# Kernel tuning notes

Measured on AMD Instinct MI355X. Metric: run time of the kernel, lower is better.

Reference implementation:

```python
import jax, jax.numpy as jnp
import numpy as np

NH, NL, NPNT = 8, 4, 4          # heads, levels, points
NQ, BS, NK, D, DFFN = 100, 8, 18, 256, 1024
SPATIAL = np.array([[92, 92], [46, 46], [23, 23], [12, 12]], np.int32)
LEN_MEM = int((SPATIAL[:, 0] * SPATIAL[:, 1]).sum())  # 11253


def _layernorm(x, g, b):
    m = x.mean(-1, keepdims=True)
    v = ((x - m) ** 2).mean(-1, keepdims=True)
    return (x - m) / jnp.sqrt(v + 1e-5) * g + b


def _mha(xq, xk, xv, in_w, in_b, out_w, out_b):
    # torch nn.MultiheadAttention semantics, inputs (S, B, D)
    S, B, d = xq.shape
    dh = d // NH
    wq, wk, wv = jnp.split(in_w, 3, axis=0)
    bq, bk, bv = jnp.split(in_b, 3, axis=0)
    def proj(x, w, b):
        return (x @ w.T + b).reshape(x.shape[0], B, NH, dh).transpose(1, 2, 0, 3)
    q = proj(xq, wq, bq) * (1.0 / np.sqrt(dh))
    k = proj(xk, wk, bk)
    v = proj(xv, wv, bv)
    att = jax.nn.softmax(jnp.einsum('bhqd,bhkd->bhqk', q, k), axis=-1)
    o = jnp.einsum('bhqk,bhkd->bhqd', att, v).transpose(2, 0, 1, 3).reshape(S, B, d)
    return o @ out_w.T + out_b


def _bilinear(v_l, loc):
    # v_l: (bs,H,W,NH,dh); loc: (bs,Lq,NH,P,2) normalized [0,1]
    # matches F.grid_sample(align_corners=False, padding_mode='zeros')
    bs, H, W, nh, dh = v_l.shape
    x = loc[..., 0] * W - 0.5
    y = loc[..., 1] * H - 0.5
    x0 = jnp.floor(x); y0 = jnp.floor(y)
    lx = x - x0; ly = y - y0
    b_idx = jnp.arange(bs)[:, None, None, None]
    h_idx = jnp.arange(nh)[None, None, :, None]
    def corner(xa, ya, w):
        valid = (xa >= 0) & (xa < W) & (ya >= 0) & (ya < H)
        xi = jnp.clip(xa, 0, W - 1).astype(jnp.int32)
        yi = jnp.clip(ya, 0, H - 1).astype(jnp.int32)
        return v_l[b_idx, yi, xi, h_idx] * (w * valid)[..., None]
    return (corner(x0, y0, (1 - lx) * (1 - ly)) + corner(x0 + 1, y0, lx * (1 - ly))
            + corner(x0, y0 + 1, (1 - lx) * ly) + corner(x0 + 1, y0 + 1, lx * ly))


def _msda(q, rp, mem, pad_mask, ss, off_w, off_b, aw_w, aw_b, val_w, val_b, outp_w, outp_b):
    bs, Lq, d = q.shape
    dh = d // NH
    value = mem @ val_w.T + val_b
    value = jnp.where(pad_mask[..., None], 0.0, value).reshape(bs, -1, NH, dh)
    off = (q @ off_w.T + off_b).reshape(bs, Lq, NH, NL, NPNT, 2)
    aw = jax.nn.softmax((q @ aw_w.T + aw_b).reshape(bs, Lq, NH, NL * NPNT), -1)
    aw = aw.reshape(bs, Lq, NH, NL, NPNT)
    wh = jnp.asarray(ss[:, ::-1].copy(), jnp.float32)  # offset normalizer (W, H)
    loc = rp[:, :, None, :, None, :] + off / wh[None, None, None, :, None, :]
    out = jnp.zeros((bs, Lq, NH, dh), q.dtype)
    start = 0
    for l in range(NL):
        H, W = int(ss[l, 0]), int(ss[l, 1])
        v_l = value[:, start:start + H * W].reshape(bs, H, W, NH, dh)
        start += H * W
        samp = _bilinear(v_l, loc[:, :, :, l])          # (bs,Lq,NH,P,dh)
        out = out + (samp * aw[:, :, :, l, :, None]).sum(3)
    return out.reshape(bs, Lq, d) @ outp_w.T + outp_b


def _forward(tgt_pose, pos, ref_points, memory, w_in_w, w_in_b, w_out_w, w_out_b,
             a_in_w, a_in_b, a_out_w, a_out_b, off_w, off_b, aw_w, aw_b,
             val_w, val_b, outp_w, outp_b, wn_g, wn_b, an_g, an_b,
             n1_g, n1_b, n2_g, n2_b, l1_w, l1_b, l2_w, l2_b,
             spatial_shapes, level_start_index, padding_mask):
    ss = np.asarray(jax.device_get(spatial_shapes))
    nq, bs, nk, d = tgt_pose.shape
    # within-group self-attn over the nk keypoint tokens.
    # NOTE: with_pos_embed mutates tgt_pose in place in the torch code, so
    # q = k = v = tgt + pos and the residual also uses tgt + pos (faithful).
    t = tgt_pose + pos
    x = t.reshape(nq * bs, nk, d).transpose(1, 0, 2)   # (nk, nq*bs, d)
    a1 = _mha(x, x, x, w_in_w, w_in_b, w_out_w, w_out_b)
    t = _layernorm(t + a1.transpose(1, 0, 2).reshape(nq, bs, nk, d), wn_g, wn_b)
    # across-group self-attn over the nq groups
    x2 = t.reshape(nq, bs * nk, d)
    a2 = _mha(x2, x2, x2, a_in_w, a_in_b, a_out_w, a_out_b)
    t = _layernorm(t + a2.reshape(nq, bs, nk, d), an_g, an_b)
    # MSDeformAttn cross-attention (in-place pos add again, faithful)
    t = t + pos
    q = t.transpose(1, 0, 2, 3).reshape(bs, nq * nk, d)
    rp = jnp.swapaxes(ref_points, 0, 1)                # (bs, nq*nk, NL, 2)
    mem = jnp.swapaxes(memory, 0, 1)                   # (bs, LEN_MEM, d)
    c = _msda(q, rp, mem, padding_mask, ss, off_w, off_b, aw_w, aw_b,
              val_w, val_b, outp_w, outp_b)
    c = c.reshape(bs, nq, nk, d).transpose(1, 0, 2, 3)
    t = _layernorm(t + c, n1_g, n1_b)
    # FFN (dropout is identity in eval)
    h = jax.nn.relu(t @ l1_w.T + l1_b)
    return _layernorm(t + (h @ l2_w.T + l2_b), n2_g, n2_b)


def setup_inputs() -> dict:
    key = jax.random.key(0)
    ks = jax.random.split(key, 16)
    p = lambda k, shape: jax.random.normal(k, shape, jnp.float32) * 0.02
    lsi = np.concatenate([[0], np.cumsum(SPATIAL[:, 0] * SPATIAL[:, 1])[:-1]]).astype(np.int32)
    return {
        'tgt_pose': jax.random.normal(ks[0], (NQ, BS, NK, D), jnp.float32),
        'pos': jax.random.normal(ks[1], (NQ, BS, NK, D), jnp.float32),
        'ref_points': jax.random.uniform(ks[2], (NQ * NK, BS, NL, 2), jnp.float32),
        'memory': jax.random.normal(ks[3], (LEN_MEM, BS, D), jnp.float32),
        'w_in_w': p(ks[4], (3 * D, D)), 'w_in_b': jnp.zeros((3 * D,)),
        'w_out_w': p(ks[5], (D, D)), 'w_out_b': jnp.zeros((D,)),
        'a_in_w': p(ks[6], (3 * D, D)), 'a_in_b': jnp.zeros((3 * D,)),
        'a_out_w': p(ks[7], (D, D)), 'a_out_b': jnp.zeros((D,)),
        'off_w': p(ks[8], (NH * NL * NPNT * 2, D)),
        'off_b': jax.random.uniform(ks[9], (NH * NL * NPNT * 2,), jnp.float32, -2.0, 2.0),
        'aw_w': p(ks[10], (NH * NL * NPNT, D)), 'aw_b': jnp.zeros((NH * NL * NPNT,)),
        'val_w': p(ks[11], (D, D)), 'val_b': jnp.zeros((D,)),
        'outp_w': p(ks[12], (D, D)), 'outp_b': jnp.zeros((D,)),
        'wn_g': jnp.ones((D,)), 'wn_b': jnp.zeros((D,)),
        'an_g': jnp.ones((D,)), 'an_b': jnp.zeros((D,)),
        'n1_g': jnp.ones((D,)), 'n1_b': jnp.zeros((D,)),
        'n2_g': jnp.ones((D,)), 'n2_b': jnp.zeros((D,)),
        'l1_w': p(ks[13], (DFFN, D)), 'l1_b': jnp.zeros((DFFN,)),
        'l2_w': p(ks[14], (D, DFFN)), 'l2_b': jnp.zeros((D,)),
        'spatial_shapes': jnp.asarray(SPATIAL),
        'level_start_index': jnp.asarray(lsi),
        'padding_mask': jnp.zeros((BS, LEN_MEM), bool),
    }


def reference(tgt_pose, pos, ref_points, memory, w_in_w, w_in_b, w_out_w, w_out_b,
              a_in_w, a_in_b, a_out_w, a_out_b, off_w, off_b, aw_w, aw_b,
              val_w, val_b, outp_w, outp_b, wn_g, wn_b, an_g, an_b,
              n1_g, n1_b, n2_g, n2_b, l1_w, l1_b, l2_w, l2_b,
              spatial_shapes, level_start_index, padding_mask):
    return _forward(tgt_pose, pos, ref_points, memory, w_in_w, w_in_b, w_out_w, w_out_b,
                    a_in_w, a_in_b, a_out_w, a_out_b, off_w, off_b, aw_w, aw_b,
                    val_w, val_b, outp_w, outp_b, wn_g, wn_b, an_g, an_b,
                    n1_g, n1_b, n2_g, n2_b, l1_w, l1_b, l2_w, l2_b,
                    spatial_shapes, level_start_index, padding_mask)
```

## Files before the change

### kernel.cpp

```cpp
#include <hip/hip_runtime.h>
#include <math.h>

#define NH_ 8
#define D_ 256
#define NK_ 18
#define NQ_ 100
#define BS_ 8
#define LQ_ 1800
#define LEN_MEM_ 11253
#define NTOK_ 14400

typedef short bf16x8 __attribute__((ext_vector_type(8)));
typedef float f32x4 __attribute__((ext_vector_type(4)));
typedef unsigned short ushort;

__device__ inline ushort f2bf(float f) {
    unsigned int u = __builtin_bit_cast(unsigned int, f);
    unsigned int r = (u + 0x7fffu + ((u >> 16) & 1u)) >> 16;
    return (ushort)r;
}
__device__ inline float bf2f(unsigned int u16) {
    unsigned int i = u16 << 16;
    return __builtin_bit_cast(float, i);
}
__device__ inline int packbf2(float a, float b) {
    return (int)f2bf(a) | ((int)f2bf(b) << 16);
}

__global__ __launch_bounds__(256)
void wcvt_kernel(const float* s0, const float* s1, const float* s2, const float* s3,
                 const float* s4, const float* s5, const float* s6, const float* s7,
                 const float* s8, const float* s9, ushort* dst) {
    const int sizes[10] = {196608,65536,196608,65536,65536,32768,65536,65536,262144,262144};
    const int offs[10]  = {0,196608,262144,458752,524288,589824,622592,688128,753664,1015808};
    int ti = blockIdx.y;
    const float* s;
    switch (ti) {
        case 0: s = s0; break; case 1: s = s1; break; case 2: s = s2; break;
        case 3: s = s3; break; case 4: s = s4; break; case 5: s = s5; break;
        case 6: s = s6; break; case 7: s = s7; break; case 8: s = s8; break;
        default: s = s9; break;
    }
    int n = sizes[ti];
    int i = (blockIdx.x * 256 + threadIdx.x) * 8;
    if (i >= n) return;
    ushort* d = dst + offs[ti] + i;
    float4 f0 = *(const float4*)(s + i);
    float4 f1 = *(const float4*)(s + i + 4);
    int4 val;
    val.x = packbf2(f0.x, f0.y);
    val.y = packbf2(f0.z, f0.w);
    val.z = packbf2(f1.x, f1.y);
    val.w = packbf2(f1.z, f1.w);
    *(int4*)d = val;
}

__global__ __launch_bounds__(256)
void addcvt_kernel(const float* __restrict__ a, const float* __restrict__ b,
                   float* __restrict__ c, ushort* __restrict__ cbf, int n4) {
    int i = blockIdx.x * blockDim.x + threadIdx.x;
    if (i >= n4) return;
    float4 av = ((const float4*)a)[i];
    float4 bv = ((const float4*)b)[i];
    float4 cv;
    cv.x = av.x + bv.x; cv.y = av.y + bv.y; cv.z = av.z + bv.z; cv.w = av.w + bv.w;
    ((float4*)c)[i] = cv;
    uint2 p;
    p.x = (unsigned int)packbf2(cv.x, cv.y);
    p.y = (unsigned int)packbf2(cv.z, cv.w);
    *(uint2*)(cbf + (size_t)i * 4) = p;
}

template<int MODE, bool RELU, bool A_F32, bool OUT_BF16>
__global__ __launch_bounds__(256)
void gemm_kernel(const void* __restrict__ Av, const ushort* __restrict__ W,
                 const float* __restrict__ bias, void* __restrict__ Cv,
                 int M, int N, int K, const unsigned char* __restrict__ mask) {
    constexpr int AST = 72;
    __shared__ ushort As[128 * AST];
    __shared__ ushort Bs[128 * AST];
    const int m0 = blockIdx.x * 128, n0 = blockIdx.y * 128;
    const int tid = threadIdx.x;
    const int w = tid >> 6, lane = tid & 63;
    const int wr = w >> 1, wc = w & 1;
    const int fr = lane & 15, hi = lane >> 4;
    f32x4 acc[4][4];
#pragma unroll
    for (int i = 0; i < 4; ++i)
#pragma unroll
        for (int j = 0; j < 4; ++j) acc[i][j] = f32x4{0.f, 0.f, 0.f, 0.f};

    const int srow = tid >> 1, shalf = tid & 1;
    long arow = 0;
    const bool avalid = (m0 + srow) < M;
    {
        int gr = m0 + srow;
        if (gr >= M) gr = M - 1;
        if (MODE == 2) {
            int b = gr / LQ_; int lq = gr - b * LQ_;
            int q = lq / NK_; int kk = lq - q * NK_;
            arow = (long)q * (BS_ * NK_) + b * NK_ + kk;
        } else {
            arow = gr;
        }
    }

    for (int k0 = 0; k0 < K; k0 += 64) {
        ushort* ad = As + srow * AST + shalf * 32;
        if (avalid) {
            if (A_F32) {
                const float* ap = (const float*)Av + arow * (long)K + k0 + shalf * 32;
#pragma unroll
                for (int i = 0; i < 4; ++i) {
                    float4 f0 = *(const float4*)(ap + i * 8);
                    float4 f1 = *(const float4*)(ap + i * 8 + 4);
                    int4 v;
                    v.x = packbf2(f0.x, f0.y); v.y = packbf2(f0.z, f0.w);
                    v.z = packbf2(f1.x, f1.y); v.w = packbf2(f1.z, f1.w);
                    *(int4*)(ad + i * 8) = v;
                }
            } else {
                const ushort* ap = (const ushort*)Av + arow * (long)K + k0 + shalf * 32;
#pragma unroll
                for (int i = 0; i < 4; ++i) *(int4*)(ad + i * 8) = *(const int4*)(ap + i * 8);
            }
        } else {
            int4 z = make_int4(0, 0, 0, 0);
#pragma unroll
            for (int i = 0; i < 4; ++i) *(int4*)(ad + i * 8) = z;
        }
        {
            const ushort* wp = W + (long)(n0 + srow) * K + k0 + shalf * 32;
            ushort* bd = Bs + srow * AST + shalf * 32;
#pragma unroll
            for (int i = 0; i < 4; ++i) *(int4*)(bd + i * 8) = *(const int4*)(wp + i * 8);
        }
        __syncthreads();
#pragma unroll
        for (int kb = 0; kb < 2; ++kb) {
            bf16x8 af[4], bfr[4];
#pragma unroll
            for (int i = 0; i < 4; ++i)
                af[i] = *(const bf16x8*)(As + (wr * 64 + i * 16 + fr) * AST + kb * 32 + hi * 8);
#pragma unroll
            for (int j = 0; j < 4; ++j)
                bfr[j] = *(const bf16x8*)(Bs + (wc * 64 + j * 16 + fr) * AST + kb * 32 + hi * 8);
#pragma unroll
            for (int i = 0; i < 4; ++i)
#pragma unroll
                for (int j = 0; j < 4; ++j)
                    acc[i][j] = __builtin_amdgcn_mfma_f32_16x16x32_bf16(af[i], bfr[j], acc[i][j], 0, 0, 0);
        }
        __syncthreads();
    }

#pragma unroll
    for (int i = 0; i < 4; ++i) {
#pragma unroll
        for (int r = 0; r < 4; ++r) {
            int gm = m0 + wr * 64 + i * 16 + hi * 4 + r;
            if (gm >= M) continue;
            long orow = gm;
            bool zero = false;
            if (MODE == 1) {
                if (mask && mask[(size_t)(gm & 7) * LEN_MEM_ + (gm >> 3)]) zero = true;
            } else if (MODE == 3) {
                int b = gm / LQ_; int lq = gm - b * LQ_;
                int q = lq / NK_; int kk = lq - q * NK_;
                orow = (long)q * (BS_ * NK_) + b * NK_ + kk;
            }
#pragma unroll
            for (int j = 0; j < 4; ++j) {
                int gn = n0 + wc * 64 + j * 16 + fr;
                float v = acc[i][j][r] + bias[gn];
                if (RELU) v = fmaxf(v, 0.f);
                if (zero) v = 0.f;
                if (OUT_BF16) ((ushort*)Cv)[orow * (long)N + gn] = f2bf(v);
                else ((float*)Cv)[orow * (long)N + gn] = v;
            }
        }
    }
}

template<int S, int SP, int HPB>
__global__ __launch_bounds__(256)
void mattn_kernel(const ushort* __restrict__ qkv, ushort* __restrict__ outb,
                  int rsG, int rsS) {
    constexpr int SPk = ((SP + 31) / 32) * 32;
    constexpr int KST = 40;
    constexpr int PST = SPk + 8;
    constexpr int NT = SP / 16;
    constexpr int NB = HPB * NT;
    constexpr int HB = 8 / HPB;
    __shared__ ushort KsA[HPB * SP * KST];
    __shared__ ushort VtA[HPB * 32 * PST];
    __shared__ ushort PA [HPB * SP * PST];

    const int tid = threadIdx.x;
    const int g = blockIdx.x / HB;
    const int hbase = (blockIdx.x % HB) * HPB;

    for (int idx = tid; idx < HPB * S * 4; idx += 256) {
        int hh = idx / (S * 4); int rem = idx - hh * (S * 4);
        int j = rem >> 2, q = rem & 3;
        const ushort* base = qkv + ((size_t)g * rsG + (size_t)j * rsS) * 768 + (hbase + hh) * 32 + q * 8;
        uint4 kv = *(const uint4*)(base + 256);
        ushort* kd = KsA + hh * (SP * KST) + j * KST + q * 8;
        *(uint2*)kd = make_uint2(kv.x, kv.y);
        *(uint2*)(kd + 4) = make_uint2(kv.z, kv.w);
        uint4 vv = *(const uint4*)(base + 512);
        ushort* vt = VtA + hh * (32 * PST) + j;
        unsigned int uu[4] = {vv.x, vv.y, vv.z, vv.w};
#pragma unroll
        for (int e = 0; e < 4; ++e) {
            vt[(q * 8 + e * 2    ) * PST] = (ushort)(uu[e] & 0xffff);
            vt[(q * 8 + e * 2 + 1) * PST] = (ushort)(uu[e] >> 16);
        }
    }
    for (int idx = tid; idx < HPB * 32 * (SPk - S); idx += 256) {
        int hh = idx / (32 * (SPk - S)); int rem = idx - hh * (32 * (SPk - S));
        int d = rem / (SPk - S); int c = S + rem - d * (SPk - S);
        VtA[hh * 32 * PST + d * PST + c] = 0;
    }
    if constexpr (SPk > SP) {
        constexpr int PW = SPk - SP;
        for (int idx = tid; idx < HPB * SP * PW; idx += 256) {
            int hh = idx / (SP * PW); int rem = idx - hh * (SP * PW);
            int rrow = rem / PW; int c = SP + rem - rrow * PW;
            PA[hh * SP * PST + rrow * PST + c] = 0;
        }
    }
    __syncthreads();

    const int wv = tid >> 6, lane = tid & 63, fr = lane & 15, hi = lane >> 4;
    for (int band = wv; band < NB; band += 4) {
        const int hh = band / NT, mb = band - (band / NT) * NT;
        const int h = hbase + hh;
        const ushort* Ks = KsA + hh * (SP * KST);
        const ushort* Vt = VtA + hh * (32 * PST);
        ushort* P = PA + hh * (SP * PST);

        int sq = mb * 16 + fr; if (sq > S - 1) sq = S - 1;
        bf16x8 qf = *(const bf16x8*)(qkv + ((size_t)g * rsG + (size_t)sq * rsS) * 768 + h * 32 + hi * 8);
        f32x4 sc[NT];
#pragma unroll
        for (int t = 0; t < NT; ++t) {
            bf16x8 kf = *(const bf16x8*)(Ks + (t * 16 + fr) * KST + hi * 8);
            sc[t] = __builtin_amdgcn_mfma_f32_16x16x32_bf16(qf, kf, f32x4{0.f, 0.f, 0.f, 0.f}, 0, 0, 0);
        }
#pragma unroll
        for (int t = 0; t < NT; ++t) {
            bool valid = (t * 16 + fr) < S;
#pragma unroll
            for (int r = 0; r < 4; ++r)
                sc[t][r] = valid ? sc[t][r] * 0.17677669529663687f : -1e30f;
        }
#pragma unroll
        for (int r = 0; r < 4; ++r) {
            float m = sc[0][r];
#pragma unroll
            for (int t = 1; t < NT; ++t) m = fmaxf(m, sc[t][r]);
            m = fmaxf(m, __shfl_xor(m, 1)); m = fmaxf(m, __shfl_xor(m, 2));
            m = fmaxf(m, __shfl_xor(m, 4)); m = fmaxf(m, __shfl_xor(m, 8));
            float e[NT]; float sum = 0.f;
#pragma unroll
            for (int t = 0; t < NT; ++t) { e[t] = __expf(sc[t][r] - m); sum += e[t]; }
            sum += __shfl_xor(sum, 1); sum += __shfl_xor(sum, 2);
            sum += __shfl_xor(sum, 4); sum += __shfl_xor(sum, 8);
            float inv = 1.f / sum;
            int row = mb * 16 + hi * 4 + r;
#pragma unroll
            for (int t = 0; t < NT; ++t)
                P[row * PST + t * 16 + fr] = f2bf(e[t] * inv);
        }
        f32x4 o0 = {0.f, 0.f, 0.f, 0.f}, o1 = {0.f, 0.f, 0.f, 0.f};
#pragma unroll
        for (int kb = 0; kb < SPk / 32; ++kb) {
            bf16x8 pf = *(const bf16x8*)(P + (mb * 16 + fr) * PST + kb * 32 + hi * 8);
            bf16x8 v0 = *(const bf16x8*)(Vt + fr * PST + kb * 32 + hi * 8);
            bf16x8 v1 = *(const bf16x8*)(Vt + (16 + fr) * PST + kb * 32 + hi * 8);
            o0 = __builtin_amdgcn_mfma_f32_16x16x32_bf16(pf, v0, o0, 0, 0, 0);
            o1 = __builtin_amdgcn_mfma_f32_16x16x32_bf16(pf, v1, o1, 0, 0, 0);
        }
#pragma unroll
        for (int r = 0; r < 4; ++r) {
            int s = mb * 16 + hi * 4 + r;
            if (s < S) {
                size_t ob = ((size_t)g * rsG + (size_t)s * rsS) * 256 + h * 32;
                outb[ob + fr] = f2bf(o0[r]);
                outb[ob + 16 + fr] = f2bf(o1[r]);
            }
        }
    }
}

__global__ __launch_bounds__(256)
void addln_kernel(const float* __restrict__ base, const float* __restrict__ delta,
                  const float* __restrict__ gamma, const float* __restrict__ beta,
                  const float* __restrict__ pos,
                  float* __restrict__ out, ushort* __restrict__ obf, int M) {
    int row = blockIdx.x * 4 + (threadIdx.x >> 6);
    int lane = threadIdx.x & 63;
    if (row >= M) return;
    const float* pb = base + (size_t)row * 256;
    const float* pd = delta + (size_t)row * 256;
    float v[4]; float s = 0.f;
#pragma unroll
    for (int i = 0; i < 4; ++i) { int c = lane + i * 64; v[i] = pb[c] + pd[c]; s += v[i]; }
#pragma unroll
    for (int off = 32; off; off >>= 1) s += __shfl_xor(s, off);
    float mean = s * (1.f / 256.f);
    float var = 0.f;
#pragma unroll
    for (int i = 0; i < 4; ++i) { float d = v[i] - mean; var += d * d; }
#pragma unroll
    for (int off = 32; off; off >>= 1) var += __shfl_xor(var, off);
    var *= (1.f / 256.f);
    float rstd = rsqrtf(var + 1e-5f);
#pragma unroll
    for (int i = 0; i < 4; ++i) {
        int c = lane + i * 64;
        float o = (v[i] - mean) * rstd * gamma[c] + beta[c];
        if (pos) o += pos[(size_t)row * 256 + c];
        out[(size_t)row * 256 + c] = o;
        if (obf) obf[(size_t)row * 256 + c] = f2bf(o);
    }
}

__global__ __launch_bounds__(256)
void msda_kernel(const float* __restrict__ offb, const float* __restrict__ aw,
                 const ushort* __restrict__ val, const float* __restrict__ refp,
                 const int* __restrict__ spatial, const int* __restrict__ lsi,
                 ushort* __restrict__ samp) {
    int unit = blockIdx.x * 16 + (threadIdx.x >> 4);
    int lane = threadIdx.x & 15;
    int lbase = (threadIdx.x & 63) & 48;
    int h = unit & 7;
    int t = unit >> 3;
    int lq = t % LQ_;
    int b = t / LQ_;

    float logit = aw[((size_t)b * LQ_ + lq) * 128 + h * 16 + lane];
    float m = logit;
    m = fmaxf(m, __shfl_xor(m, 1)); m = fmaxf(m, __shfl_xor(m, 2));
    m = fmaxf(m, __shfl_xor(m, 4)); m = fmaxf(m, __shfl_xor(m, 8));
    float e = __expf(logit - m);
    float sum = e;
    sum += __shfl_xor(sum, 1); sum += __shfl_xor(sum, 2);
    sum += __shfl_xor(sum, 4); sum += __shfl_xor(sum, 8);
    float wnorm = e / sum;

    const float* offp = offb + ((size_t)b * LQ_ + lq) * 256 + h * 32;
    float2 myoff = ((const float2*)offp)[lane];

    float acc0 = 0.f, acc1 = 0.f;
#pragma unroll
    for (int lvl = 0; lvl < 4; ++lvl) {
        int H = spatial[lvl * 2], W = spatial[lvl * 2 + 1];
        int st = lsi[lvl];
        float rpx = refp[(((size_t)lq * BS_ + b) * 4 + lvl) * 2 + 0];
        float rpy = refp[(((size_t)lq * BS_ + b) * 4 + lvl) * 2 + 1];
        const ushort* vb = val + ((size_t)st * 8 + b) * 256 + h * 32 + lane * 2;
        float fW = (float)W, fH = (float)H;
#pragma unroll
        for (int p = 0; p < 4; ++p) {
            int pi = lvl * 4 + p;
            float ox = __shfl(myoff.x, lbase + pi);
            float oy = __shfl(myoff.y, lbase + pi);
            float wpt = __shfl(wnorm, lbase + pi);
            float x = rpx * fW + ox - 0.5f;
            float y = rpy * fH + oy - 0.5f;
            float x0f = floorf(x), y0f = floorf(y);
            float lx = x - x0f, ly = y - y0f;
            int x0 = (int)x0f, y0 = (int)y0f;
            int xc0 = min(max(x0, 0), W - 1), xc1 = min(max(x0 + 1, 0), W - 1);
            int yc0 = min(max(y0, 0), H - 1), yc1 = min(max(y0 + 1, 0), H - 1);
            float vx0 = (x0 >= 0 && x0 < W) ? 1.f : 0.f;
            float vx1 = (x0 >= -1 && x0 + 1 < W) ? 1.f : 0.f;
            float vy0 = (y0 >= 0 && y0 < H) ? 1.f : 0.f;
            float vy1 = (y0 >= -1 && y0 + 1 < H) ? 1.f : 0.f;
            float w00 = wpt * (1.f - lx) * (1.f - ly) * vx0 * vy0;
            float w10 = wpt * lx * (1.f - ly) * vx1 * vy0;
            float w01 = wpt * (1.f - lx) * ly * vx0 * vy1;
            float w11 = wpt * lx * ly * vx1 * vy1;
            unsigned int u00 = *(const unsigned int*)(vb + ((size_t)(yc0 * W + xc0) * 8) * 256);
            unsigned int u10 = *(const unsigned int*)(vb + ((size_t)(yc0 * W + xc1) * 8) * 256);
            unsigned int u01 = *(const unsigned int*)(vb + ((size_t)(yc1 * W + xc0) * 8) * 256);
            unsigned int u11 = *(const unsigned int*)(vb + ((size_t)(yc1 * W + xc1) * 8) * 256);
            acc0 += w00 * bf2f(u00 & 0xffff) + w10 * bf2f(u10 & 0xffff)
                  + w01 * bf2f(u01 & 0xffff) + w11 * bf2f(u11 & 0xffff);
            acc1 += w00 * bf2f(u00 >> 16) + w10 * bf2f(u10 >> 16)
                  + w01 * bf2f(u01 >> 16) + w11 * bf2f(u11 >> 16);
        }
    }
    size_t o = ((size_t)b * LQ_ + lq) * 256 + h * 32 + lane * 2;
    *(unsigned int*)(samp + o) = (unsigned int)packbf2(acc0, acc1);
}

extern "C" void kernel_launch(void* const* d_in, const int* in_sizes, int n_in,
                              void* d_out, int out_size, void* d_ws, size_t ws_size,
                              hipStream_t stream) {
    const float* tgt     = (const float*)d_in[0];
    const float* pos     = (const float*)d_in[1];
    const float* refp    = (const float*)d_in[2];
    const float* memory  = (const float*)d_in[3];
    const float* w_in_w  = (const float*)d_in[4];
    const float* w_in_b  = (const float*)d_in[5];
    const float* w_out_w = (const float*)d_in[6];
    const float* w_out_b = (const float*)d_in[7];
    const float* a_in_w  = (const float*)d_in[8];
    const float* a_in_b  = (const float*)d_in[9];
    const float* a_out_w = (const float*)d_in[10];
    const float* a_out_b = (const float*)d_in[11];
    const float* off_w   = (const float*)d_in[12];
    const float* off_b   = (const float*)d_in[13];
    const float* aw_w    = (const float*)d_in[14];
    const float* aw_b    = (const float*)d_in[15];
    const float* val_w   = (const float*)d_in[16];
    const float* val_b   = (const float*)d_in[17];
    const float* outp_w  = (const float*)d_in[18];
    const float* outp_b  = (const float*)d_in[19];
    const float* wn_g    = (const float*)d_in[20];
    const float* wn_b    = (const float*)d_in[21];
    const float* an_g    = (const float*)d_in[22];
    const float* an_b    = (const float*)d_in[23];
    const float* n1_g    = (const float*)d_in[24];
    const float* n1_b    = (const float*)d_in[25];
    const float* n2_g    = (const float*)d_in[26];
    const float* n2_b    = (const float*)d_in[27];
    const float* l1_w    = (const float*)d_in[28];
    const float* l1_b    = (const float*)d_in[29];
    const float* l2_w    = (const float*)d_in[30];
    const float* l2_b    = (const float*)d_in[31];
    const int*   spatial = (const int*)d_in[32];
    const int*   lsi     = (const int*)d_in[33];
    const unsigned char* pmask = (const unsigned char*)d_in[34];
    float* out = (float*)d_out;

    float*  T      = (float*)d_ws;
    ushort* Tbf    = (ushort*)(T + 3686400);
    ushort* B16    = Tbf + 3686400;
    ushort* CBbf   = B16 + 11059200;
    ushort* VALbf  = CBbf + 3686400;
    ushort* SAMPbf = VALbf + 23046144;
    ushort* Hbf    = SAMPbf + 3686400;
    ushort* WB     = Hbf + 14745600;
    float*  OFF    = (float*)(WB + 1277952);
    float*  AW     = OFF + 3686400;

    ushort* WB_win  = WB + 0;
    ushort* WB_wout = WB + 196608;
    ushort* WB_ain  = WB + 262144;
    ushort* WB_aout = WB + 458752;
    ushort* WB_off  = WB + 524288;
    ushort* WB_aw   = WB + 589824;
    ushort* WB_val  = WB + 622592;
    ushort* WB_outp = WB + 688128;
    ushort* WB_l1   = WB + 753664;
    ushort* WB_l2   = WB + 1015808;

    const int n4 = NTOK_ * 256 / 4;

    wcvt_kernel<<<dim3(128, 10), 256, 0, stream>>>(
        w_in_w, w_out_w, a_in_w, a_out_w, off_w, aw_w, val_w, outp_w, l1_w, l2_w, WB);
    addcvt_kernel<<<n4 / 256, 256, 0, stream>>>(tgt, pos, T, Tbf, n4);
    gemm_kernel<0, false, false, true><<<dim3(113, 6), 256, 0, stream>>>(
        Tbf, WB_win, w_in_b, B16, NTOK_, 768, 256, nullptr);
    mattn_kernel<18, 32, 4><<<800 * 2, 256, 0, stream>>>(B16, CBbf, 18, 1);
    gemm_kernel<0, false, false, false><<<dim3(113, 2), 256, 0, stream>>>(
        CBbf, WB_wout, w_out_b, OFF, NTOK_, 256, 256, nullptr);
    addln_kernel<<<NTOK_ / 4, 256, 0, stream>>>(T, OFF, wn_g, wn_b, nullptr, T, Tbf, NTOK_);
    gemm_kernel<0, false, false, true><<<dim3(113, 6), 256, 0, stream>>>(
        Tbf, WB_ain, a_in_b, B16, NTOK_, 768, 256, nullptr);
    mattn_kernel<100, 112, 1><<<144 * 8, 256, 0, stream>>>(B16, CBbf, 1, 144);
    gemm_kernel<0, false, false, false><<<dim3(113, 2), 256, 0, stream>>>(
        CBbf, WB_aout, a_out_b, OFF, NTOK_, 256, 256, nullptr);
    addln_kernel<<<NTOK_ / 4, 256, 0, stream>>>(T, OFF, an_g, an_b, pos, T, Tbf, NTOK_);
    gemm_kernel<1, false, true, true><<<dim3(704, 2), 256, 0, stream>>>(
        memory, WB_val, val_b, VALbf, 90024, 256, 256, pmask);
    gemm_kernel<2, false, false, false><<<dim3(113, 2), 256, 0, stream>>>(
        Tbf, WB_off, off_b, OFF, NTOK_, 256, 256, nullptr);
    gemm_kernel<2, false, false, false><<<dim3(113, 1), 256, 0, stream>>>(
        Tbf, WB_aw, aw_b, AW, NTOK_, 128, 256, nullptr);
    msda_kernel<<<NTOK_ * 8 / 16, 256, 0, stream>>>(OFF, AW, VALbf, refp, spatial, lsi, SAMPbf);
    gemm_kernel<3, false, false, false><<<dim3(113, 2), 256, 0, stream>>>(
        SAMPbf, WB_outp, outp_b, OFF, NTOK_, 256, 256, nullptr);
    addln_kernel<<<NTOK_ / 4, 256, 0, stream>>>(T, OFF, n1_g, n1_b, nullptr, T, Tbf, NTOK_);
    gemm_kernel<0, true, false, true><<<dim3(113, 8), 256, 0, stream>>>(
        Tbf, WB_l1, l1_b, Hbf, NTOK_, 1024, 256, nullptr);
    gemm_kernel<0, false, false, false><<<dim3(113, 2), 256, 0, stream>>>(
        Hbf, WB_l2, l2_b, OFF, NTOK_, 256, 1024, nullptr);
    addln_kernel<<<NTOK_ / 4, 256, 0, stream>>>(T, OFF, n2_g, n2_b, nullptr, out, nullptr, NTOK_);
}
```

Measured before the change: 361.1 us.

## Add weight-stationary K=256 GEMM kernel with swizzled LDS and register-streamed A

Adds a GEMM specialised for K=256 that loads the full 256xBN weight slice into XOR-swizzled shared memory once per block. Each wave then streams its 16 rows of A straight from global memory into MFMA registers, with a one-step prefetch and no A staging in LDS and no per-k-step barriers. All K=256 GEMMs use it, including the fp32 memory value projection with padding mask (256-wide N, 8 waves) and the permuted-row modes. The old tiled kernel is trimmed to serve only the K=1024 FFN output GEMM. The cost is that weights are reloaded per block, and each block covers only 64-128 rows, so global traffic for W rises.

```diff
diff --git a/kernel.cpp b/kernel.cpp
--- a/kernel.cpp
+++ b/kernel.cpp
@@ -71,6 +71,106 @@
     *(uint2*)(cbf + (size_t)i * 4) = p;
 }
 
+template<int MODE, bool RELU, bool A_F32, bool OUT_BF16, int BN, int WAVES>
+__global__ __launch_bounds__(WAVES * 64)
+void gemmw_kernel(const void* __restrict__ Av, const ushort* __restrict__ W,
+                  const float* __restrict__ bias, void* __restrict__ Cv,
+                  int M, int N, const unsigned char* __restrict__ mask) {
+    constexpr int K = 256;
+    constexpr int NT = BN / 16;
+    __shared__ ushort Ws[32 * BN * 8];
+    const int tid = threadIdx.x;
+    const int m0 = blockIdx.x * (WAVES * 16);
+    const int n0 = blockIdx.y * BN;
+
+    for (int c = tid; c < 32 * BN; c += WAVES * 64) {
+        int kc = c & 31, n = c >> 5;
+        int dst = kc * BN + (n ^ (kc & 7));
+        *(int4*)(Ws + dst * 8) = *(const int4*)(W + (long)(n0 + n) * K + kc * 8);
+    }
+    __syncthreads();
+
+    const int wv = tid >> 6, lane = tid & 63, fr = lane & 15, hi = lane >> 4;
+    const int wm0 = m0 + wv * 16;
+    int gr = wm0 + fr;
+    if (gr > M - 1) gr = M - 1;
+    long arow;
+    if (MODE == 2) {
+        int b = gr / LQ_; int lq = gr - b * LQ_;
+        int q = lq / NK_; int kk = lq - q * NK_;
+        arow = (long)q * (BS_ * NK_) + b * NK_ + kk;
+    } else {
+        arow = gr;
+    }
+
+    f32x4 acc[NT];
+#pragma unroll
+    for (int t = 0; t < NT; ++t) acc[t] = f32x4{0.f, 0.f, 0.f, 0.f};
+
+    if (A_F32) {
+        const float* ap = (const float*)Av + arow * (long)K + hi * 8;
+        float4 p0 = *(const float4*)ap;
+        float4 p1 = *(const float4*)(ap + 4);
+#pragma unroll
+        for (int ks = 0; ks < 8; ++ks) {
+            int4 v;
+            v.x = packbf2(p0.x, p0.y); v.y = packbf2(p0.z, p0.w);
+            v.z = packbf2(p1.x, p1.y); v.w = packbf2(p1.z, p1.w);
+            bf16x8 cur = __builtin_bit_cast(bf16x8, v);
+            if (ks < 7) {
+                p0 = *(const float4*)(ap + (ks + 1) * 32);
+                p1 = *(const float4*)(ap + (ks + 1) * 32 + 4);
+            }
+            const int kc = ks * 4 + hi;
+            const ushort* wb = Ws + ((kc * BN) + (fr ^ (kc & 7))) * 8;
+#pragma unroll
+            for (int t = 0; t < NT; ++t) {
+                bf16x8 wf = *(const bf16x8*)(wb + t * 128);
+                acc[t] = __builtin_amdgcn_mfma_f32_16x16x32_bf16(cur, wf, acc[t], 0, 0, 0);
+            }
+        }
+    } else {
+        const ushort* ap = (const ushort*)Av + arow * (long)K + hi * 8;
+        bf16x8 afrag = *(const bf16x8*)ap;
+#pragma unroll
+        for (int ks = 0; ks < 8; ++ks) {
+            bf16x8 cur = afrag;
+            if (ks < 7) afrag = *(const bf16x8*)(ap + (ks + 1) * 32);
+            const int kc = ks * 4 + hi;
+            const ushort* wb = Ws + ((kc * BN) + (fr ^ (kc & 7))) * 8;
+#pragma unroll
+            for (int t = 0; t < NT; ++t) {
+                bf16x8 wf = *(const bf16x8*)(wb + t * 128);
+                acc[t] = __builtin_amdgcn_mfma_f32_16x16x32_bf16(cur, wf, acc[t], 0, 0, 0);
+            }
+        }
+    }
+
+#pragma unroll
+    for (int r = 0; r < 4; ++r) {
+        int gm = wm0 + hi * 4 + r;
+        if (gm >= M) continue;
+        long orow = gm;
+        bool zero = false;
+        if (MODE == 1) {
+            if (mask && mask[(size_t)(gm & 7) * LEN_MEM_ + (gm >> 3)]) zero = true;
+        } else if (MODE == 3) {
+            int b = gm / LQ_; int lq = gm - b * LQ_;
+            int q = lq / NK_; int kk = lq - q * NK_;
+            orow = (long)q * (BS_ * NK_) + b * NK_ + kk;
+        }
+#pragma unroll
+        for (int t = 0; t < NT; ++t) {
+            int gn = n0 + t * 16 + fr;
+            float v = acc[t][r] + bias[gn];
+            if (RELU) v = fmaxf(v, 0.f);
+            if (zero) v = 0.f;
+            if (OUT_BF16) ((ushort*)Cv)[orow * (long)N + gn] = f2bf(v);
+            else ((float*)Cv)[orow * (long)N + gn] = v;
+        }
+    }
+}
+
 template<int MODE, bool RELU, bool A_F32, bool OUT_BF16>
 __global__ __launch_bounds__(256)
 void gemm_kernel(const void* __restrict__ Av, const ushort* __restrict__ W,
@@ -96,34 +196,15 @@
     {
         int gr = m0 + srow;
         if (gr >= M) gr = M - 1;
-        if (MODE == 2) {
-            int b = gr / LQ_; int lq = gr - b * LQ_;
-            int q = lq / NK_; int kk = lq - q * NK_;
-            arow = (long)q * (BS_ * NK_) + b * NK_ + kk;
-        } else {
-            arow = gr;
-        }
+        arow = gr;
     }
 
     for (int k0 = 0; k0 < K; k0 += 64) {
         ushort* ad = As + srow * AST + shalf * 32;
         if (avalid) {
-            if (A_F32) {
-                const float* ap = (const float*)Av + arow * (long)K + k0 + shalf * 32;
-#pragma unroll
-                for (int i = 0; i < 4; ++i) {
-                    float4 f0 = *(const float4*)(ap + i * 8);
-                    float4 f1 = *(const float4*)(ap + i * 8 + 4);
-                    int4 v;
-                    v.x = packbf2(f0.x, f0.y); v.y = packbf2(f0.z, f0.w);
-                    v.z = packbf2(f1.x, f1.y); v.w = packbf2(f1.z, f1.w);
-                    *(int4*)(ad + i * 8) = v;
-                }
-            } else {
-                const ushort* ap = (const ushort*)Av + arow * (long)K + k0 + shalf * 32;
-#pragma unroll
-                for (int i = 0; i < 4; ++i) *(int4*)(ad + i * 8) = *(const int4*)(ap + i * 8);
-            }
+            const ushort* ap = (const ushort*)Av + arow * (long)K + k0 + shalf * 32;
+#pragma unroll
+            for (int i = 0; i < 4; ++i) *(int4*)(ad + i * 8) = *(const int4*)(ap + i * 8);
         } else {
             int4 z = make_int4(0, 0, 0, 0);
 #pragma unroll
@@ -160,23 +241,13 @@
         for (int r = 0; r < 4; ++r) {
             int gm = m0 + wr * 64 + i * 16 + hi * 4 + r;
             if (gm >= M) continue;
-            long orow = gm;
-            bool zero = false;
-            if (MODE == 1) {
-                if (mask && mask[(size_t)(gm & 7) * LEN_MEM_ + (gm >> 3)]) zero = true;
-            } else if (MODE == 3) {
-                int b = gm / LQ_; int lq = gm - b * LQ_;
-                int q = lq / NK_; int kk = lq - q * NK_;
-                orow = (long)q * (BS_ * NK_) + b * NK_ + kk;
-            }
 #pragma unroll
             for (int j = 0; j < 4; ++j) {
                 int gn = n0 + wc * 64 + j * 16 + fr;
                 float v = acc[i][j][r] + bias[gn];
                 if (RELU) v = fmaxf(v, 0.f);
-                if (zero) v = 0.f;
-                if (OUT_BF16) ((ushort*)Cv)[orow * (long)N + gn] = f2bf(v);
-                else ((float*)Cv)[orow * (long)N + gn] = v;
+                if (OUT_BF16) ((ushort*)Cv)[(long)gm * N + gn] = f2bf(v);
+                else ((float*)Cv)[(long)gm * N + gn] = v;
             }
         }
     }
@@ -464,30 +535,30 @@
     wcvt_kernel<<<dim3(128, 10), 256, 0, stream>>>(
         w_in_w, w_out_w, a_in_w, a_out_w, off_w, aw_w, val_w, outp_w, l1_w, l2_w, WB);
     addcvt_kernel<<<n4 / 256, 256, 0, stream>>>(tgt, pos, T, Tbf, n4);
-    gemm_kernel<0, false, false, true><<<dim3(113, 6), 256, 0, stream>>>(
-        Tbf, WB_win, w_in_b, B16, NTOK_, 768, 256, nullptr);
+    gemmw_kernel<0, false, false, true, 128, 4><<<dim3(225, 6), 256, 0, stream>>>(
+        Tbf, WB_win, w_in_b, B16, NTOK_, 768, nullptr);
     mattn_kernel<18, 32, 4><<<800 * 2, 256, 0, stream>>>(B16, CBbf, 18, 1);
-    gemm_kernel<0, false, false, false><<<dim3(113, 2), 256, 0, stream>>>(
-        CBbf, WB_wout, w_out_b, OFF, NTOK_, 256, 256, nullptr);
+    gemmw_kernel<0, false, false, false, 128, 4><<<dim3(225, 2), 256, 0, stream>>>(
+        CBbf, WB_wout, w_out_b, OFF, NTOK_, 256, nullptr);
     addln_kernel<<<NTOK_ / 4, 256, 0, stream>>>(T, OFF, wn_g, wn_b, nullptr, T, Tbf, NTOK_);
-    gemm_kernel<0, false, false, true><<<dim3(113, 6), 256, 0, stream>>>(
-        Tbf, WB_ain, a_in_b, B16, NTOK_, 768, 256, nullptr);
+    gemmw_kernel<0, false, false, true, 128, 4><<<dim3(225, 6), 256, 0, stream>>>(
+        Tbf, WB_ain, a_in_b, B16, NTOK_, 768, nullptr);
     mattn_kernel<100, 112, 1><<<144 * 8, 256, 0, stream>>>(B16, CBbf, 1, 144);
-    gemm_kernel<0, false, false, false><<<dim3(113, 2), 256, 0, stream>>>(
-        CBbf, WB_aout, a_out_b, OFF, NTOK_, 256, 256, nullptr);
+    gemmw_kernel<0, false, false, false, 128, 4><<<dim3(225, 2), 256, 0, stream>>>(
+        CBbf, WB_aout, a_out_b, OFF, NTOK_, 256, nullptr);
     addln_kernel<<<NTOK_ / 4, 256, 0, stream>>>(T, OFF, an_g, an_b, pos, T, Tbf, NTOK_);
-    gemm_kernel<1, false, true, true><<<dim3(704, 2), 256, 0, stream>>>(
-        memory, WB_val, val_b, VALbf, 90024, 256, 256, pmask);
-    gemm_kernel<2, false, false, false><<<dim3(113, 2), 256, 0, stream>>>(
-        Tbf, WB_off, off_b, OFF, NTOK_, 256, 256, nullptr);
-    gemm_kernel<2, false, false, false><<<dim3(113, 1), 256, 0, stream>>>(
-        Tbf, WB_aw, aw_b, AW, NTOK_, 128, 256, nullptr);
+    gemmw_kernel<1, false, true, true, 256, 8><<<dim3(704, 1), 512, 0, stream>>>(
+        memory, WB_val, val_b, VALbf, 90024, 256, pmask);
+    gemmw_kernel<2, false, false, false, 128, 4><<<dim3(225, 2), 256, 0, stream>>>(
+        Tbf, WB_off, off_b, OFF, NTOK_, 256, nullptr);
+    gemmw_kernel<2, false, false, false, 128, 4><<<dim3(225, 1), 256, 0, stream>>>(
+        Tbf, WB_aw, aw_b, AW, NTOK_, 128, nullptr);
     msda_kernel<<<NTOK_ * 8 / 16, 256, 0, stream>>>(OFF, AW, VALbf, refp, spatial, lsi, SAMPbf);
-    gemm_kernel<3, false, false, false><<<dim3(113, 2), 256, 0, stream>>>(
-        SAMPbf, WB_outp, outp_b, OFF, NTOK_, 256, 256, nullptr);
+    gemmw_kernel<3, false, false, false, 128, 4><<<dim3(225, 2), 256, 0, stream>>>(
+        SAMPbf, WB_outp, outp_b, OFF, NTOK_, 256, nullptr);
     addln_kernel<<<NTOK_ / 4, 256, 0, stream>>>(T, OFF, n1_g, n1_b, nullptr, T, Tbf, NTOK_);
-    gemm_kernel<0, true, false, true><<<dim3(113, 8), 256, 0, stream>>>(
-        Tbf, WB_l1, l1_b, Hbf, NTOK_, 1024, 256, nullptr);
+    gemmw_kernel<0, true, false, true, 128, 4><<<dim3(225, 8), 256, 0, stream>>>(
+        Tbf, WB_l1, l1_b, Hbf, NTOK_, 1024, nullptr);
     gemm_kernel<0, false, false, false><<<dim3(113, 2), 256, 0, stream>>>(
         Hbf, WB_l2, l2_b, OFF, NTOK_, 256, 1024, nullptr);
     addln_kernel<<<NTOK_ / 4, 256, 0, stream>>>(T, OFF, n2_g, n2_b, nullptr, out, nullptr, NTOK_);
```

New measurement: 377.1 us. +4.4%, slower.
